# Kernel tuning notes

Measured on AMD Instinct MI355X. Metric: run time of the kernel, lower is better.

## Reference

```python
import jax, jax.numpy as jnp
import numpy as np

HIDDEN = 4096
INTER = 11008
BATCH, SEQ = 2, 2048


def _ternary(key, shape):
    # BitNet b1.58 ternary weights in {-1, 0, +1}
    return jax.random.randint(key, shape, -1, 2).astype(jnp.float32)


def setup_inputs() -> dict:
    key = jax.random.key(0)
    kx, kg, ku, kd = jax.random.split(key, 4)
    x = jax.random.normal(kx, (BATCH, SEQ, HIDDEN), dtype=jnp.float32)
    gate_w = _ternary(kg, (INTER, HIDDEN))
    up_w = _ternary(ku, (INTER, HIDDEN))
    down_w = _ternary(kd, (HIDDEN, INTER))
    # per-tensor absmean scales (dequant factors)
    gate_scale = jnp.float32(0.02)
    up_scale = jnp.float32(0.02)
    down_scale = jnp.float32(0.02)
    return {"x": x, "gate_w": gate_w, "up_w": up_w, "down_w": down_w,
            "gate_scale": gate_scale, "up_scale": up_scale, "down_scale": down_scale}


def reference(x, gate_w, up_w, down_w, gate_scale, up_scale, down_scale):
    # QuantizedLinear: y = (x @ W_q^T) * scale, W_q ternary, bias=False
    gate = jnp.einsum('bsh,ih->bsi', x, gate_w) * gate_scale
    up = jnp.einsum('bsh,ih->bsi', x, up_w) * up_scale
    inter = jax.nn.silu(gate) * up  # SwiGLU
    out = jnp.einsum('bsi,hi->bsh', inter, down_w) * down_scale
    return out
```

## Files before the change

kernel.cpp:

```cpp
#include <hip/hip_runtime.h>


typedef short short8 __attribute__((ext_vector_type(8)));
typedef float f32x4 __attribute__((ext_vector_type(4)));
typedef float fvec4 __attribute__((ext_vector_type(4)));
typedef unsigned short usvec4 __attribute__((ext_vector_type(4)));

__device__ __forceinline__ unsigned short f2bf(float f) {
    unsigned int u = __float_as_uint(f);
    u += 0x7FFFu + ((u >> 16) & 1u);
    return (unsigned short)(u >> 16);
}

__global__ void cvt_f32_bf16(const fvec4* __restrict__ src,
                             usvec4* __restrict__ dst, long n4) {
    long i = (long)blockIdx.x * blockDim.x + threadIdx.x;
    if (i < n4) {
        fvec4 v = __builtin_nontemporal_load(src + i);
        usvec4 o;
        o.x = f2bf(v.x); o.y = f2bf(v.y); o.z = f2bf(v.z); o.w = f2bf(v.w);
        dst[i] = o;
    }
}

__global__ void cvt2_f32_bf16_ilv(const fvec4* __restrict__ s0,
                                  const fvec4* __restrict__ s1,
                                  usvec4* __restrict__ d, long n4) {
    long i = (long)blockIdx.x * blockDim.x + threadIdx.x;
    if (i < n4) {
        long j = i >> 10;
        long c = i & 1023;
        long Rg = ((j & ~15L) << 1) | (j & 15);
        fvec4 a = __builtin_nontemporal_load(s0 + i);
        fvec4 b = __builtin_nontemporal_load(s1 + i);
        usvec4 oa, ob;
        oa.x = f2bf(a.x); oa.y = f2bf(a.y); oa.z = f2bf(a.z); oa.w = f2bf(a.w);
        ob.x = f2bf(b.x); ob.y = f2bf(b.y); ob.z = f2bf(b.z); ob.w = f2bf(b.w);
        d[Rg * 1024 + c] = oa;
        d[(Rg + 16) * 1024 + c] = ob;
    }
}

#define GLOBAL_TO_LDS(gp, lp)                                                  \
    __builtin_amdgcn_global_load_lds(                                          \
        (__attribute__((address_space(1))) const void*)(gp),                   \
        (__attribute__((address_space(3))) void*)(lp), 16, 0, 0)

#define BAR() __builtin_amdgcn_s_barrier()
#define SCHEDB() __builtin_amdgcn_sched_barrier(0)
#define LGKM(n) do { asm volatile("s_waitcnt lgkmcnt(" #n ")" ::: "memory"); SCHEDB(); } while (0)
#define VMW(n) asm volatile("s_waitcnt vmcnt(" #n ")" ::: "memory")

__device__ __forceinline__ void remap_block(int gy, int& bx, int& by) {
    int nwg = gy << 4;
    int orig = blockIdx.y * 16 + blockIdx.x;
    int q = nwg >> 3, r = nwg & 7;
    int xcd = orig & 7, lid = orig >> 3;
    int wg = (xcd < r ? xcd * (q + 1) : r * (q + 1) + (xcd - r) * q) + lid;
    bx = wg & 15;
    by = wg >> 4;
}

#define KITER(KT_, BFC, BFN, TOK4, PF_, RA_)                                   \
  do {                                                                         \
    LGKM(4);                        \
    __builtin_amdgcn_s_setprio(1);                                             \
    _Pragma("unroll") for (int mi = 0; mi < 4; ++mi)                           \
      _Pragma("unroll") for (int ni = 0; ni < 4; ++ni)                         \
        acc[mi][ni] = __builtin_amdgcn_mfma_f32_16x16x32_bf16(                 \
            ah0[mi], BFC[ni], acc[mi][ni], 0, 0, 0);                           \
    __builtin_amdgcn_s_setprio(0);                                             \
    SCHEDB();                                                                  \
    if (TOK4) { VMW(4); } else { VMW(0); }                                     \
    BAR();                                   \
    if (RA_) {                                                                 \
      const unsigned short* Aq = lds + ((((KT_) + 1) & 3) << 13);              \
      const unsigned short* Bq = lds + 32768 + ((((KT_) + 1) & 3) << 13);      \
      _Pragma("unroll") for (int i = 0; i < 4; ++i)                            \
        ah0[i] = *(const short8*)(Aq + aoff + i * 512);                        \
      _Pragma("unroll") for (int n = 0; n < 4; ++n)                            \
        BFN[n] = *(const short8*)(Bq + boff + n * 512);                        \
    }                                                                          \
    if (PF_) {                                                                 \
      unsigned short* Aw = lds + ((((KT_) + 3) & 3) << 13);                    \
      unsigned short* Bw = lds + 32768 + ((((KT_) + 3) & 3) << 13);            \
      GLOBAL_TO_LDS(pa0, Aw + t * 8);                                          \
      GLOBAL_TO_LDS(pa1, Aw + 4096 + t * 8);                                   \
      GLOBAL_TO_LDS(pb0, Bw + t * 8);                                          \
      GLOBAL_TO_LDS(pb1, Bw + 4096 + t * 8);                                   \
      pa0 += 32; pa1 += 32; pb0 += 32; pb1 += 32;                              \
    }                                                                          \
    SCHEDB();                                                                  \
    if (RA_) { LGKM(8); } else { LGKM(0); }   \
    __builtin_amdgcn_s_setprio(1);                                             \
    _Pragma("unroll") for (int mi = 0; mi < 4; ++mi)                           \
      _Pragma("unroll") for (int ni = 0; ni < 4; ++ni)                         \
        acc[4 + mi][ni] = __builtin_amdgcn_mfma_f32_16x16x32_bf16(             \
            ah1[mi], BFC[ni], acc[4 + mi][ni], 0, 0, 0);                       \
    __builtin_amdgcn_s_setprio(0);                                             \
    SCHEDB();                                                                  \
    if (RA_) {          \
      const unsigned short* Aq = lds + ((((KT_) + 1) & 3) << 13);              \
      _Pragma("unroll") for (int i = 0; i < 4; ++i)                            \
        ah1[i] = *(const short8*)(Aq + aoff + (4 + i) * 512);                  \
      SCHEDB();                                                                \
    }                                                                          \
  } while (0)

#define KPRO()                                                                 \
  do {                                                                         \
    _Pragma("unroll") for (int s = 0; s < 3; ++s) {                            \
      unsigned short* Aw = lds + (s << 13);                                    \
      unsigned short* Bw = lds + 32768 + (s << 13);                            \
      GLOBAL_TO_LDS(pa0, Aw + t * 8);                                          \
      GLOBAL_TO_LDS(pa1, Aw + 4096 + t * 8);                                   \
      GLOBAL_TO_LDS(pb0, Bw + t * 8);                                          \
      GLOBAL_TO_LDS(pb1, Bw + 4096 + t * 8);                                   \
      pa0 += 32; pa1 += 32; pb0 += 32; pb1 += 32;                              \
    }                                                                          \
    VMW(8); BAR();                     \
    _Pragma("unroll") for (int i = 0; i < 4; ++i)                              \
      ah0[i] = *(const short8*)(lds + aoff + i * 512);                         \
    _Pragma("unroll") for (int n = 0; n < 4; ++n)                              \
      bfA[n] = *(const short8*)(lds + 32768 + boff + n * 512);                 \
    _Pragma("unroll") for (int i = 0; i < 4; ++i)                              \
      ah1[i] = *(const short8*)(lds + aoff + (4 + i) * 512);                   \
    SCHEDB();                                                                  \
  } while (0)

#define KLOOP()                                                                \
  do {                                                                         \
    for (int kt = 0; kt < Kt - 4; kt += 2) {                                   \
      KITER(kt, bfA, bfB, 1, 1, 1);                                            \
      KITER(kt + 1, bfB, bfA, 1, 1, 1);                                        \
    }                                                                          \
    KITER(Kt - 4, bfA, bfB, 1, 1, 1);                                          \
    KITER(Kt - 3, bfB, bfA, 1, 0, 1);                                          \
    KITER(Kt - 2, bfA, bfB, 0, 0, 1);                                          \
    KITER(Kt - 1, bfB, bfA, 0, 0, 0);                                          \
  } while (0)

__global__ __launch_bounds__(512, 2)
void gemm1_swiglu(const unsigned short* __restrict__ Xb,
                  const unsigned short* __restrict__ Wc,
                  unsigned short* __restrict__ inter,
                  const float* __restrict__ gs_p,
                  const float* __restrict__ us_p,
                  int K, int I, int n0, int gy) {
    extern __shared__ unsigned short lds[];

    int bx, by;
    remap_block(gy, bx, by);

    const int t = threadIdx.x;
    const int lane = t & 63;
    const int wid = t >> 6;
    const int wm = (wid >> 2) * 128;
    const int wn = (wid & 3) * 64;
    const int fr = lane & 15;
    const int ca = (((lane >> 4) ^ ((fr >> 1) & 3)) << 3);

    const int m_base = bx * 256;
    const long b_row0 = (long)by * 256;

    const int colsw = (((t & 3) ^ ((t >> 3) & 3)) << 3);
    const unsigned short* pa0 = Xb + (size_t)(m_base + (t >> 2)) * K + colsw;
    const unsigned short* pa1 = pa0 + (size_t)128 * K;
    const unsigned short* pb0 = Wc + (size_t)(b_row0 + (t >> 2)) * K + colsw;
    const unsigned short* pb1 = pb0 + (size_t)128 * K;

    f32x4 acc[8][4];
    const f32x4 z = {0.0f, 0.0f, 0.0f, 0.0f};
#pragma unroll
    for (int i = 0; i < 8; ++i)
#pragma unroll
        for (int j = 0; j < 4; ++j) acc[i][j] = z;

    const int aoff = (wm + fr) * 32 + ca;
    const int boff = (wn + fr) * 32 + ca;
    const int Kt = K >> 5;

    short8 ah0[4], ah1[4], bfA[4], bfB[4];

    KPRO();
    KLOOP();

    const float gsc = *gs_p;
    const float usc = *us_p;
    const int row0 = m_base + wm + ((lane >> 4) << 2);
    const int col0 = n0 + by * 128 + (wn >> 1) + fr;
#pragma unroll
    for (int mi = 0; mi < 8; ++mi)
#pragma unroll
        for (int p = 0; p < 2; ++p)
#pragma unroll
            for (int r = 0; r < 4; ++r) {
                float g = acc[mi][2 * p][r] * gsc;
                float u = acc[mi][2 * p + 1][r] * usc;
                float s = g / (1.0f + __expf(-g));
                inter[(size_t)(row0 + mi * 16 + r) * I + (col0 + p * 16)] =
                    f2bf(s * u);
            }
}

__global__ __launch_bounds__(512, 2)
void gemm2_down(const unsigned short* __restrict__ Ab,
                const unsigned short* __restrict__ Dw,
                float* __restrict__ out,
                const float* __restrict__ ds_p,
                int K, int H, int n0, int gy) {
    extern __shared__ unsigned short lds[];

    int bx, by;
    remap_block(gy, bx, by);

    const int t = threadIdx.x;
    const int lane = t & 63;
    const int wid = t >> 6;
    const int wm = (wid >> 2) * 128;
    const int wn = (wid & 3) * 64;
    const int fr = lane & 15;
    const int ca = (((lane >> 4) ^ ((fr >> 1) & 3)) << 3);

    const int m_base = bx * 256;
    const long b_row0 = (long)by * 256;

    const int colsw = (((t & 3) ^ ((t >> 3) & 3)) << 3);
    const unsigned short* pa0 = Ab + (size_t)(m_base + (t >> 2)) * K + colsw;
    const unsigned short* pa1 = pa0 + (size_t)128 * K;
    const unsigned short* pb0 = Dw + (size_t)(b_row0 + (t >> 2)) * K + colsw;
    const unsigned short* pb1 = pb0 + (size_t)128 * K;

    f32x4 acc[8][4];
    const f32x4 z = {0.0f, 0.0f, 0.0f, 0.0f};
#pragma unroll
    for (int i = 0; i < 8; ++i)
#pragma unroll
        for (int j = 0; j < 4; ++j) acc[i][j] = z;

    const int aoff = (wm + fr) * 32 + ca;
    const int boff = (wn + fr) * 32 + ca;
    const int Kt = K >> 5;

    short8 ah0[4], ah1[4], bfA[4], bfB[4];

    KPRO();
    KLOOP();

    const float dsc = *ds_p;
    const int row0 = m_base + wm + ((lane >> 4) << 2);
    const int col0 = n0 + by * 256 + wn + fr;
#pragma unroll
    for (int mi = 0; mi < 8; ++mi)
#pragma unroll
        for (int ni = 0; ni < 4; ++ni)
#pragma unroll
            for (int r = 0; r < 4; ++r)
                out[(size_t)(row0 + mi * 16 + r) * H + (col0 + ni * 16)] =
                    acc[mi][ni][r] * dsc;
}

extern "C" void kernel_launch(void* const* d_in, const int* in_sizes, int n_in,
                              void* d_out, int out_size, void* d_ws, size_t ws_size,
                              hipStream_t stream) {
    (void)in_sizes; (void)n_in; (void)out_size;
    const float* x  = (const float*)d_in[0];
    const float* gw = (const float*)d_in[1];
    const float* uw = (const float*)d_in[2];
    const float* dw = (const float*)d_in[3];
    const float* gs = (const float*)d_in[4];
    const float* us = (const float*)d_in[5];
    const float* ds = (const float*)d_in[6];
    float* out = (float*)d_out;

    const long M = 4096;
    const long Kh = 4096;
    const long I = 11008;
    const long H = 4096;

    (void)hipFuncSetAttribute(reinterpret_cast<const void*>(gemm1_swiglu),
                              hipFuncAttributeMaxDynamicSharedMemorySize, 131072);
    (void)hipFuncSetAttribute(reinterpret_cast<const void*>(gemm2_down),
                              hipFuncAttributeMaxDynamicSharedMemorySize, 131072);

    char* ws = (char*)d_ws;
    unsigned short* Xb = (unsigned short*)ws;
    unsigned short* inter = (unsigned short*)(ws + M * Kh * 2);
    const size_t used = (size_t)M * Kh * 2 + (size_t)M * I * 2;
    if (ws_size < used + 2 * (size_t)256 * Kh * 2) return;
    char* wbuf = ws + used;
    const size_t avail = ws_size - used;

    {
        long n4 = M * Kh / 4;
        cvt_f32_bf16<<<dim3((unsigned)((n4 + 255) / 256)), dim3(256), 0, stream>>>(
            (const fvec4*)x, (usvec4*)Xb, n4);
    }

    long mr1 = (long)(avail / ((size_t)2 * Kh * 2));
    mr1 = (mr1 / 128) * 128;
    if (mr1 > I) mr1 = I;
    if (mr1 < 128) mr1 = 128;
    unsigned short* Wc = (unsigned short*)wbuf;
    for (long n0 = 0; n0 < I; n0 += mr1) {
        long rc = (I - n0 < mr1) ? (I - n0) : mr1;
        long e4 = rc * Kh / 4;
        unsigned cb = (unsigned)((e4 + 255) / 256);
        cvt2_f32_bf16_ilv<<<dim3(cb), dim3(256), 0, stream>>>(
            (const fvec4*)(gw + n0 * Kh), (const fvec4*)(uw + n0 * Kh),
            (usvec4*)Wc, e4);
        unsigned gy = (unsigned)(rc / 128);
        gemm1_swiglu<<<dim3(16, gy), dim3(512), 131072, stream>>>(
            Xb, Wc, inter, gs, us, (int)Kh, (int)I, (int)n0, (int)gy);
    }

    long mr2 = (long)(avail / ((size_t)I * 2));
    mr2 = (mr2 / 256) * 256;
    if (mr2 > H) mr2 = H;
    if (mr2 < 256) mr2 = 256;
    unsigned short* Wd = (unsigned short*)wbuf;
    for (long h0 = 0; h0 < H; h0 += mr2) {
        long rc = (H - h0 < mr2) ? (H - h0) : mr2;
        long e4 = rc * I / 4;
        unsigned cb = (unsigned)((e4 + 255) / 256);
        cvt_f32_bf16<<<dim3(cb), dim3(256), 0, stream>>>(
            (const fvec4*)(dw + h0 * I), (usvec4*)Wd, e4);
        unsigned gy = (unsigned)(rc / 256);
        gemm2_down<<<dim3(16, gy), dim3(512), 131072, stream>>>(
            inter, Wd, out, ds, (int)I, (int)H, (int)h0, (int)gy);
    }
}
```

Baseline: 1.394 ms.

## Fuse fp32-to-bf16 weight conversion into GEMM mainloops via register staging

Drops the separate weight conversion kernels and chunked launch loops. Both GEMMs now load fp32 weights straight into registers, truncate them to bf16 by packing the high halves, and write them to LDS one stage ahead, while activations still use direct global-to-LDS loads. This removes the bf16 weight round-trip through memory and the extra launches, but each block now reads twice the weight bytes, converts by truncation instead of round-to-nearest (exact for ternary weights), and changes the wait-count scheduling. The x conversion kernel becomes grid-stride with a fixed grid.

Result: slower. 2.053 ms (+47.2%).

```diff
diff --git a/kernel.cpp b/kernel.cpp
--- a/kernel.cpp
+++ b/kernel.cpp
@@ -5,6 +5,7 @@
 typedef float f32x4 __attribute__((ext_vector_type(4)));
 typedef float fvec4 __attribute__((ext_vector_type(4)));
 typedef unsigned short usvec4 __attribute__((ext_vector_type(4)));
+typedef unsigned int u32x4 __attribute__((ext_vector_type(4)));
 
 __device__ __forceinline__ unsigned short f2bf(float f) {
     unsigned int u = __float_as_uint(f);
@@ -12,32 +13,18 @@
     return (unsigned short)(u >> 16);
 }
 
+__device__ __forceinline__ unsigned pkbf(unsigned a, unsigned b) {
+    return (a >> 16) | (b & 0xFFFF0000u);
+}
+
 __global__ void cvt_f32_bf16(const fvec4* __restrict__ src,
                              usvec4* __restrict__ dst, long n4) {
-    long i = (long)blockIdx.x * blockDim.x + threadIdx.x;
-    if (i < n4) {
+    long stride = (long)gridDim.x * blockDim.x;
+    for (long i = (long)blockIdx.x * blockDim.x + threadIdx.x; i < n4; i += stride) {
         fvec4 v = __builtin_nontemporal_load(src + i);
         usvec4 o;
         o.x = f2bf(v.x); o.y = f2bf(v.y); o.z = f2bf(v.z); o.w = f2bf(v.w);
         dst[i] = o;
-    }
-}
-
-__global__ void cvt2_f32_bf16_ilv(const fvec4* __restrict__ s0,
-                                  const fvec4* __restrict__ s1,
-                                  usvec4* __restrict__ d, long n4) {
-    long i = (long)blockIdx.x * blockDim.x + threadIdx.x;
-    if (i < n4) {
-        long j = i >> 10;
-        long c = i & 1023;
-        long Rg = ((j & ~15L) << 1) | (j & 15);
-        fvec4 a = __builtin_nontemporal_load(s0 + i);
-        fvec4 b = __builtin_nontemporal_load(s1 + i);
-        usvec4 oa, ob;
-        oa.x = f2bf(a.x); oa.y = f2bf(a.y); oa.z = f2bf(a.z); oa.w = f2bf(a.w);
-        ob.x = f2bf(b.x); ob.y = f2bf(b.y); ob.z = f2bf(b.z); ob.w = f2bf(b.w);
-        d[Rg * 1024 + c] = oa;
-        d[(Rg + 16) * 1024 + c] = ob;
     }
 }
 
@@ -61,7 +48,7 @@
     by = wg >> 4;
 }
 
-#define KITER(KT_, BFC, BFN, TOK4, PF_, RA_)                                   \
+#define KITER(KT_, BFC, BFN, WSRC, WDST, VM_, MID_, WR_, LD_, RA_)             \
   do {                                                                         \
     LGKM(4);                        \
     __builtin_amdgcn_s_setprio(1);                                             \
@@ -71,8 +58,30 @@
             ah0[mi], BFC[ni], acc[mi][ni], 0, 0, 0);                           \
     __builtin_amdgcn_s_setprio(0);                                             \
     SCHEDB();                                                                  \
-    if (TOK4) { VMW(4); } else { VMW(0); }                                     \
-    BAR();                                   \
+    VMW(VM_);                     \
+    BAR();                                                                     \
+    if (LD_) {                                                                 \
+      WDST[0] = pq0[0]; WDST[1] = pq0[1];                                      \
+      WDST[2] = pq1[0]; WDST[3] = pq1[1];                                      \
+      pq0 += 8; pq1 += 8;                                                      \
+      SCHEDB();                                                                \
+      unsigned short* Aw = lds + ((((KT_) + 3) & 3) << 13);                    \
+      GLOBAL_TO_LDS(pa0, Aw + t * 8);                                          \
+      GLOBAL_TO_LDS(pa1, Aw + 4096 + t * 8);                                   \
+      pa0 += 32; pa1 += 32;                                                    \
+      SCHEDB();                                                                \
+    }                                                                          \
+    if (WR_) {                                                                 \
+      unsigned short* Bw = lds + 32768 + ((((KT_) + 2) & 3) << 13);            \
+      u32x4 lo, hi;                                                            \
+      lo.x = pkbf(WSRC[0].x, WSRC[0].y); lo.y = pkbf(WSRC[0].z, WSRC[0].w);    \
+      lo.z = pkbf(WSRC[1].x, WSRC[1].y); lo.w = pkbf(WSRC[1].z, WSRC[1].w);    \
+      hi.x = pkbf(WSRC[2].x, WSRC[2].y); hi.y = pkbf(WSRC[2].z, WSRC[2].w);    \
+      hi.z = pkbf(WSRC[3].x, WSRC[3].y); hi.w = pkbf(WSRC[3].z, WSRC[3].w);    \
+      *(u32x4*)(Bw + t * 8) = lo;                                              \
+      *(u32x4*)(Bw + 4096 + t * 8) = hi;                                       \
+      SCHEDB();                                                                \
+    }                                                                          \
     if (RA_) {                                                                 \
       const unsigned short* Aq = lds + ((((KT_) + 1) & 3) << 13);              \
       const unsigned short* Bq = lds + 32768 + ((((KT_) + 1) & 3) << 13);      \
@@ -81,17 +90,7 @@
       _Pragma("unroll") for (int n = 0; n < 4; ++n)                            \
         BFN[n] = *(const short8*)(Bq + boff + n * 512);                        \
     }                                                                          \
-    if (PF_) {                                                                 \
-      unsigned short* Aw = lds + ((((KT_) + 3) & 3) << 13);                    \
-      unsigned short* Bw = lds + 32768 + ((((KT_) + 3) & 3) << 13);            \
-      GLOBAL_TO_LDS(pa0, Aw + t * 8);                                          \
-      GLOBAL_TO_LDS(pa1, Aw + 4096 + t * 8);                                   \
-      GLOBAL_TO_LDS(pb0, Bw + t * 8);                                          \
-      GLOBAL_TO_LDS(pb1, Bw + 4096 + t * 8);                                   \
-      pa0 += 32; pa1 += 32; pb0 += 32; pb1 += 32;                              \
-    }                                                                          \
-    SCHEDB();                                                                  \
-    if (RA_) { LGKM(8); } else { LGKM(0); }   \
+    LGKM(MID_);                                     \
     __builtin_amdgcn_s_setprio(1);                                             \
     _Pragma("unroll") for (int mi = 0; mi < 4; ++mi)                           \
       _Pragma("unroll") for (int ni = 0; ni < 4; ++ni)                         \
@@ -99,7 +98,7 @@
             ah1[mi], BFC[ni], acc[4 + mi][ni], 0, 0, 0);                       \
     __builtin_amdgcn_s_setprio(0);                                             \
     SCHEDB();                                                                  \
-    if (RA_) {          \
+    if (RA_) {                                                                 \
       const unsigned short* Aq = lds + ((((KT_) + 1) & 3) << 13);              \
       _Pragma("unroll") for (int i = 0; i < 4; ++i)                            \
         ah1[i] = *(const short8*)(Aq + aoff + (4 + i) * 512);                  \
@@ -109,16 +108,39 @@
 
 #define KPRO()                                                                 \
   do {                                                                         \
+    wP0[0] = pq0[0]; wP0[1] = pq0[1]; wP0[2] = pq1[0]; wP0[3] = pq1[1];        \
+    pq0 += 8; pq1 += 8;                                                        \
+    wP1[0] = pq0[0]; wP1[1] = pq0[1]; wP1[2] = pq1[0]; wP1[3] = pq1[1];        \
+    pq0 += 8; pq1 += 8;                                                        \
+    qA[0] = pq0[0]; qA[1] = pq0[1]; qA[2] = pq1[0]; qA[3] = pq1[1];            \
+    pq0 += 8; pq1 += 8;                                                        \
+    SCHEDB();                                                                  \
     _Pragma("unroll") for (int s = 0; s < 3; ++s) {                            \
       unsigned short* Aw = lds + (s << 13);                                    \
-      unsigned short* Bw = lds + 32768 + (s << 13);                            \
       GLOBAL_TO_LDS(pa0, Aw + t * 8);                                          \
       GLOBAL_TO_LDS(pa1, Aw + 4096 + t * 8);                                   \
-      GLOBAL_TO_LDS(pb0, Bw + t * 8);                                          \
-      GLOBAL_TO_LDS(pb1, Bw + 4096 + t * 8);                                   \
-      pa0 += 32; pa1 += 32; pb0 += 32; pb1 += 32;                              \
-    }                                                                          \
-    VMW(8); BAR();                     \
+      pa0 += 32; pa1 += 32;                                                    \
+    }                                                                          \
+    VMW(0);                                                                    \
+    {                                                                          \
+      unsigned short* Bw = lds + 32768;                                        \
+      u32x4 lo, hi;                                                            \
+      lo.x = pkbf(wP0[0].x, wP0[0].y); lo.y = pkbf(wP0[0].z, wP0[0].w);        \
+      lo.z = pkbf(wP0[1].x, wP0[1].y); lo.w = pkbf(wP0[1].z, wP0[1].w);        \
+      hi.x = pkbf(wP0[2].x, wP0[2].y); hi.y = pkbf(wP0[2].z, wP0[2].w);        \
+      hi.z = pkbf(wP0[3].x, wP0[3].y); hi.w = pkbf(wP0[3].z, wP0[3].w);        \
+      *(u32x4*)(Bw + t * 8) = lo;                                              \
+      *(u32x4*)(Bw + 4096 + t * 8) = hi;                                       \
+      Bw = lds + 32768 + 8192;                                                 \
+      lo.x = pkbf(wP1[0].x, wP1[0].y); lo.y = pkbf(wP1[0].z, wP1[0].w);        \
+      lo.z = pkbf(wP1[1].x, wP1[1].y); lo.w = pkbf(wP1[1].z, wP1[1].w);        \
+      hi.x = pkbf(wP1[2].x, wP1[2].y); hi.y = pkbf(wP1[2].z, wP1[2].w);        \
+      hi.z = pkbf(wP1[3].x, wP1[3].y); hi.w = pkbf(wP1[3].z, wP1[3].w);        \
+      *(u32x4*)(Bw + t * 8) = lo;                                              \
+      *(u32x4*)(Bw + 4096 + t * 8) = hi;                                       \
+    }                                                                          \
+    LGKM(0);                                                                   \
+    BAR();                                                                     \
     _Pragma("unroll") for (int i = 0; i < 4; ++i)                              \
       ah0[i] = *(const short8*)(lds + aoff + i * 512);                         \
     _Pragma("unroll") for (int n = 0; n < 4; ++n)                              \
@@ -130,23 +152,25 @@
 
 #define KLOOP()                                                                \
   do {                                                                         \
-    for (int kt = 0; kt < Kt - 4; kt += 2) {                                   \
-      KITER(kt, bfA, bfB, 1, 1, 1);                                            \
-      KITER(kt + 1, bfB, bfA, 1, 1, 1);                                        \
-    }                                                                          \
-    KITER(Kt - 4, bfA, bfB, 1, 1, 1);                                          \
-    KITER(Kt - 3, bfB, bfA, 1, 0, 1);                                          \
-    KITER(Kt - 2, bfA, bfB, 0, 0, 1);                                          \
-    KITER(Kt - 1, bfB, bfA, 0, 0, 0);                                          \
+    int kt = 0;                                                                \
+    for (; kt < Kt - 4; kt += 2) {                                             \
+      KITER(kt, bfA, bfB, qA, qB, 2, 10, 1, 1, 1);                             \
+      KITER(kt + 1, bfB, bfA, qB, qA, 2, 10, 1, 1, 1);                         \
+    }                                                                          \
+    KITER(kt, bfA, bfB, qA, qB, 2, 10, 1, 1, 1); ++kt;               \
+    KITER(kt, bfB, bfA, qB, qA, 2, 10, 1, 0, 1); ++kt;               \
+    KITER(kt, bfA, bfB, qA, qB, 0, 8, 0, 0, 1); ++kt;                \
+    KITER(kt, bfB, bfA, qB, qA, 0, 0, 0, 0, 0);                      \
   } while (0)
 
 __global__ __launch_bounds__(512, 2)
 void gemm1_swiglu(const unsigned short* __restrict__ Xb,
-                  const unsigned short* __restrict__ Wc,
+                  const float* __restrict__ Gw,
+                  const float* __restrict__ Uw,
                   unsigned short* __restrict__ inter,
                   const float* __restrict__ gs_p,
                   const float* __restrict__ us_p,
-                  int K, int I, int n0, int gy) {
+                  int K, int I, int gy) {
     extern __shared__ unsigned short lds[];
 
     int bx, by;
@@ -161,13 +185,17 @@
     const int ca = (((lane >> 4) ^ ((fr >> 1) & 3)) << 3);
 
     const int m_base = bx * 256;
-    const long b_row0 = (long)by * 256;
-
-    const int colsw = (((t & 3) ^ ((t >> 3) & 3)) << 3);
-    const unsigned short* pa0 = Xb + (size_t)(m_base + (t >> 2)) * K + colsw;
+
+    const int g = (t & 3) ^ ((t >> 3) & 3);
+    const int rl = t >> 2;
+    const unsigned short* pa0 = Xb + (size_t)(m_base + rl) * K + g * 8;
     const unsigned short* pa1 = pa0 + (size_t)128 * K;
-    const unsigned short* pb0 = Wc + (size_t)(b_row0 + (t >> 2)) * K + colsw;
-    const unsigned short* pb1 = pb0 + (size_t)128 * K;
+
+    const int cg = by * 256 + rl;
+    const float* wbase = ((cg >> 4) & 1) ? Uw : Gw;
+    const int srow = ((cg >> 5) << 4) + (cg & 15);
+    const u32x4* pq0 = (const u32x4*)(wbase + (size_t)srow * K) + 2 * g;
+    const u32x4* pq1 = pq0 + (size_t)16 * K;
 
     f32x4 acc[8][4];
     const f32x4 z = {0.0f, 0.0f, 0.0f, 0.0f};
@@ -181,6 +209,7 @@
     const int Kt = K >> 5;
 
     short8 ah0[4], ah1[4], bfA[4], bfB[4];
+    u32x4 qA[4], qB[4], wP0[4], wP1[4];
 
     KPRO();
     KLOOP();
@@ -188,27 +217,27 @@
     const float gsc = *gs_p;
     const float usc = *us_p;
     const int row0 = m_base + wm + ((lane >> 4) << 2);
-    const int col0 = n0 + by * 128 + (wn >> 1) + fr;
+    const int col0 = by * 128 + (wn >> 1) + fr;
 #pragma unroll
     for (int mi = 0; mi < 8; ++mi)
 #pragma unroll
         for (int p = 0; p < 2; ++p)
 #pragma unroll
             for (int r = 0; r < 4; ++r) {
-                float g = acc[mi][2 * p][r] * gsc;
-                float u = acc[mi][2 * p + 1][r] * usc;
-                float s = g / (1.0f + __expf(-g));
+                float gg = acc[mi][2 * p][r] * gsc;
+                float uu = acc[mi][2 * p + 1][r] * usc;
+                float s = gg / (1.0f + __expf(-gg));
                 inter[(size_t)(row0 + mi * 16 + r) * I + (col0 + p * 16)] =
-                    f2bf(s * u);
+                    f2bf(s * uu);
             }
 }
 
 __global__ __launch_bounds__(512, 2)
 void gemm2_down(const unsigned short* __restrict__ Ab,
-                const unsigned short* __restrict__ Dw,
+                const float* __restrict__ Dw,
                 float* __restrict__ out,
                 const float* __restrict__ ds_p,
-                int K, int H, int n0, int gy) {
+                int K, int H, int gy) {
     extern __shared__ unsigned short lds[];
 
     int bx, by;
@@ -225,11 +254,13 @@
     const int m_base = bx * 256;
     const long b_row0 = (long)by * 256;
 
-    const int colsw = (((t & 3) ^ ((t >> 3) & 3)) << 3);
-    const unsigned short* pa0 = Ab + (size_t)(m_base + (t >> 2)) * K + colsw;
+    const int g = (t & 3) ^ ((t >> 3) & 3);
+    const int rl = t >> 2;
+    const unsigned short* pa0 = Ab + (size_t)(m_base + rl) * K + g * 8;
     const unsigned short* pa1 = pa0 + (size_t)128 * K;
-    const unsigned short* pb0 = Dw + (size_t)(b_row0 + (t >> 2)) * K + colsw;
-    const unsigned short* pb1 = pb0 + (size_t)128 * K;
+
+    const u32x4* pq0 = (const u32x4*)(Dw + (size_t)(b_row0 + rl) * K) + 2 * g;
+    const u32x4* pq1 = pq0 + (size_t)32 * K;
 
     f32x4 acc[8][4];
     const f32x4 z = {0.0f, 0.0f, 0.0f, 0.0f};
@@ -243,13 +274,14 @@
     const int Kt = K >> 5;
 
     short8 ah0[4], ah1[4], bfA[4], bfB[4];
+    u32x4 qA[4], qB[4], wP0[4], wP1[4];
 
     KPRO();
     KLOOP();
 
     const float dsc = *ds_p;
     const int row0 = m_base + wm + ((lane >> 4) << 2);
-    const int col0 = n0 + by * 256 + wn + fr;
+    const int col0 = by * 256 + wn + fr;
 #pragma unroll
     for (int mi = 0; mi < 8; ++mi)
 #pragma unroll
@@ -285,48 +317,19 @@
 
     char* ws = (char*)d_ws;
     unsigned short* Xb = (unsigned short*)ws;
-    unsigned short* inter = (unsigned short*)(ws + M * Kh * 2);
+    unsigned short* inter = (unsigned short*)(ws + (size_t)M * Kh * 2);
     const size_t used = (size_t)M * Kh * 2 + (size_t)M * I * 2;
-    if (ws_size < used + 2 * (size_t)256 * Kh * 2) return;
-    char* wbuf = ws + used;
-    const size_t avail = ws_size - used;
+    if (ws_size < used) return;
 
     {
         long n4 = M * Kh / 4;
-        cvt_f32_bf16<<<dim3((unsigned)((n4 + 255) / 256)), dim3(256), 0, stream>>>(
+        cvt_f32_bf16<<<dim3(2048), dim3(256), 0, stream>>>(
             (const fvec4*)x, (usvec4*)Xb, n4);
     }
 
-    long mr1 = (long)(avail / ((size_t)2 * Kh * 2));
-    mr1 = (mr1 / 128) * 128;
-    if (mr1 > I) mr1 = I;
-    if (mr1 < 128) mr1 = 128;
-    unsigned short* Wc = (unsigned short*)wbuf;
-    for (long n0 = 0; n0 < I; n0 += mr1) {
-        long rc = (I - n0 < mr1) ? (I - n0) : mr1;
-        long e4 = rc * Kh / 4;
-        unsigned cb = (unsigned)((e4 + 255) / 256);
-        cvt2_f32_bf16_ilv<<<dim3(cb), dim3(256), 0, stream>>>(
-            (const fvec4*)(gw + n0 * Kh), (const fvec4*)(uw + n0 * Kh),
-            (usvec4*)Wc, e4);
-        unsigned gy = (unsigned)(rc / 128);
-        gemm1_swiglu<<<dim3(16, gy), dim3(512), 131072, stream>>>(
-            Xb, Wc, inter, gs, us, (int)Kh, (int)I, (int)n0, (int)gy);
-    }
-
-    long mr2 = (long)(avail / ((size_t)I * 2));
-    mr2 = (mr2 / 256) * 256;
-    if (mr2 > H) mr2 = H;
-    if (mr2 < 256) mr2 = 256;
-    unsigned short* Wd = (unsigned short*)wbuf;
-    for (long h0 = 0; h0 < H; h0 += mr2) {
-        long rc = (H - h0 < mr2) ? (H - h0) : mr2;
-        long e4 = rc * I / 4;
-        unsigned cb = (unsigned)((e4 + 255) / 256);
-        cvt_f32_bf16<<<dim3(cb), dim3(256), 0, stream>>>(
-            (const fvec4*)(dw + h0 * I), (usvec4*)Wd, e4);
-        unsigned gy = (unsigned)(rc / 256);
-        gemm2_down<<<dim3(16, gy), dim3(512), 131072, stream>>>(
-            inter, Wd, out, ds, (int)I, (int)H, (int)h0, (int)gy);
-    }
-}
+    gemm1_swiglu<<<dim3(16, 86), dim3(512), 131072, stream>>>(
+        Xb, gw, uw, inter, gs, us, (int)Kh, (int)I, 86);
+
+    gemm2_down<<<dim3(16, 16), dim3(512), 131072, stream>>>(
+        inter, dw, out, ds, (int)I, (int)H, 16);
+}
```

## Restructure GEMM main loop into 64-wide K groups with split prefetch schedule

Applied to the files above, without the earlier changes.

Replaces the per-32-K iteration pipeline with a group that processes two 32-wide K chunks at once, splitting the MFMA work into four 4x2 quadrants interleaved with LDS fragment loads and staggered global-to-LDS prefetches of A and B. The intent is to give each MFMA burst more independent work and overlap LDS reads and async copies better, at the cost of many more barriers per group and higher register use. The conversion kernels are also changed to grid-stride loops with a fixed grid of 2048 blocks.

Measured after the change: 1.379 ms. Within noise of the previous version (-1.1%).

```diff
diff --git a/kernel.cpp b/kernel.cpp
--- a/kernel.cpp
+++ b/kernel.cpp
@@ -14,8 +14,8 @@
 
 __global__ void cvt_f32_bf16(const fvec4* __restrict__ src,
                              usvec4* __restrict__ dst, long n4) {
-    long i = (long)blockIdx.x * blockDim.x + threadIdx.x;
-    if (i < n4) {
+    long stride = (long)gridDim.x * blockDim.x;
+    for (long i = (long)blockIdx.x * blockDim.x + threadIdx.x; i < n4; i += stride) {
         fvec4 v = __builtin_nontemporal_load(src + i);
         usvec4 o;
         o.x = f2bf(v.x); o.y = f2bf(v.y); o.z = f2bf(v.z); o.w = f2bf(v.w);
@@ -26,8 +26,8 @@
 __global__ void cvt2_f32_bf16_ilv(const fvec4* __restrict__ s0,
                                   const fvec4* __restrict__ s1,
                                   usvec4* __restrict__ d, long n4) {
-    long i = (long)blockIdx.x * blockDim.x + threadIdx.x;
-    if (i < n4) {
+    long stride = (long)gridDim.x * blockDim.x;
+    for (long i = (long)blockIdx.x * blockDim.x + threadIdx.x; i < n4; i += stride) {
         long j = i >> 10;
         long c = i & 1023;
         long Rg = ((j & ~15L) << 1) | (j & 15);
@@ -61,83 +61,119 @@
     by = wg >> 4;
 }
 
-#define KITER(KT_, BFC, BFN, TOK4, PF_, RA_)                                   \
-  do {                                                                         \
-    LGKM(4);                        \
-    __builtin_amdgcn_s_setprio(1);                                             \
-    _Pragma("unroll") for (int mi = 0; mi < 4; ++mi)                           \
-      _Pragma("unroll") for (int ni = 0; ni < 4; ++ni)                         \
-        acc[mi][ni] = __builtin_amdgcn_mfma_f32_16x16x32_bf16(                 \
-            ah0[mi], BFC[ni], acc[mi][ni], 0, 0, 0);                           \
-    __builtin_amdgcn_s_setprio(0);                                             \
-    SCHEDB();                                                                  \
-    if (TOK4) { VMW(4); } else { VMW(0); }                                     \
-    BAR();                                   \
-    if (RA_) {                                                                 \
-      const unsigned short* Aq = lds + ((((KT_) + 1) & 3) << 13);              \
-      const unsigned short* Bq = lds + 32768 + ((((KT_) + 1) & 3) << 13);      \
-      _Pragma("unroll") for (int i = 0; i < 4; ++i)                            \
-        ah0[i] = *(const short8*)(Aq + aoff + i * 512);                        \
-      _Pragma("unroll") for (int n = 0; n < 4; ++n)                            \
-        BFN[n] = *(const short8*)(Bq + boff + n * 512);                        \
-    }                                                                          \
-    if (PF_) {                                                                 \
-      unsigned short* Aw = lds + ((((KT_) + 3) & 3) << 13);                    \
-      unsigned short* Bw = lds + 32768 + ((((KT_) + 3) & 3) << 13);            \
-      GLOBAL_TO_LDS(pa0, Aw + t * 8);                                          \
-      GLOBAL_TO_LDS(pa1, Aw + 4096 + t * 8);                                   \
-      GLOBAL_TO_LDS(pb0, Bw + t * 8);                                          \
-      GLOBAL_TO_LDS(pb1, Bw + 4096 + t * 8);                                   \
-      pa0 += 32; pa1 += 32; pb0 += 32; pb1 += 32;                              \
-    }                                                                          \
-    SCHEDB();                                                                  \
-    if (RA_) { LGKM(8); } else { LGKM(0); }   \
-    __builtin_amdgcn_s_setprio(1);                                             \
-    _Pragma("unroll") for (int mi = 0; mi < 4; ++mi)                           \
-      _Pragma("unroll") for (int ni = 0; ni < 4; ++ni)                         \
-        acc[4 + mi][ni] = __builtin_amdgcn_mfma_f32_16x16x32_bf16(             \
-            ah1[mi], BFC[ni], acc[4 + mi][ni], 0, 0, 0);                       \
-    __builtin_amdgcn_s_setprio(0);                                             \
-    SCHEDB();                                                                  \
-    if (RA_) {          \
-      const unsigned short* Aq = lds + ((((KT_) + 1) & 3) << 13);              \
-      _Pragma("unroll") for (int i = 0; i < 4; ++i)                            \
-        ah1[i] = *(const short8*)(Aq + aoff + (4 + i) * 512);                  \
-      SCHEDB();                                                                \
-    }                                                                          \
+#define MFMA16(AH, BH, MH, NH)                                                \
+  do {                                                                        \
+    __builtin_amdgcn_s_setprio(1);                                            \
+    _Pragma("unroll") for (int kk = 0; kk < 2; ++kk)                          \
+      _Pragma("unroll") for (int mi = 0; mi < 4; ++mi)                        \
+        _Pragma("unroll") for (int ni = 0; ni < 2; ++ni)                      \
+          acc[(MH)*4+mi][(NH)*2+ni] =                                         \
+              __builtin_amdgcn_mfma_f32_16x16x32_bf16(                        \
+                  AH[kk*4+mi], BH[kk*2+ni], acc[(MH)*4+mi][(NH)*2+ni],        \
+                  0, 0, 0);                                                   \
+    __builtin_amdgcn_s_setprio(0);                                            \
+    SCHEDB();                                                                 \
   } while (0)
 
-#define KPRO()                                                                 \
-  do {                                                                         \
-    _Pragma("unroll") for (int s = 0; s < 3; ++s) {                            \
-      unsigned short* Aw = lds + (s << 13);                                    \
-      unsigned short* Bw = lds + 32768 + (s << 13);                            \
-      GLOBAL_TO_LDS(pa0, Aw + t * 8);                                          \
-      GLOBAL_TO_LDS(pa1, Aw + 4096 + t * 8);                                   \
-      GLOBAL_TO_LDS(pb0, Bw + t * 8);                                          \
-      GLOBAL_TO_LDS(pb1, Bw + 4096 + t * 8);                                   \
-      pa0 += 32; pa1 += 32; pb0 += 32; pb1 += 32;                              \
-    }                                                                          \
-    VMW(8); BAR();                     \
-    _Pragma("unroll") for (int i = 0; i < 4; ++i)                              \
-      ah0[i] = *(const short8*)(lds + aoff + i * 512);                         \
-    _Pragma("unroll") for (int n = 0; n < 4; ++n)                              \
-      bfA[n] = *(const short8*)(lds + 32768 + boff + n * 512);                 \
-    _Pragma("unroll") for (int i = 0; i < 4; ++i)                              \
-      ah1[i] = *(const short8*)(lds + aoff + (4 + i) * 512);                   \
-    SCHEDB();                                                                  \
+#define KGROUP(C0, C1, SA, SB, TOK)                                           \
+  do {                                                                        \
+         \
+    { const unsigned short* Aq0 = lds + (C0) * 8192;                          \
+      const unsigned short* Aq1 = lds + (C1) * 8192;                          \
+      const unsigned short* Bq0 = lds + 32768 + (C0) * 8192;                  \
+      const unsigned short* Bq1 = lds + 32768 + (C1) * 8192;                  \
+      _Pragma("unroll") for (int mi = 0; mi < 4; ++mi) {                      \
+        a0[mi]     = *(const short8*)(Aq0 + aoff + mi * 512);                 \
+        a0[4 + mi] = *(const short8*)(Aq1 + aoff + mi * 512);                 \
+      }                                                                       \
+      _Pragma("unroll") for (int ni = 0; ni < 2; ++ni) {                      \
+        b0[ni]     = *(const short8*)(Bq0 + boff + ni * 512);                 \
+        b0[2 + ni] = *(const short8*)(Bq1 + boff + ni * 512);                 \
+      }                                                                       \
+    }                                                                         \
+    if (SA) {                                                                 \
+      GLOBAL_TO_LDS(pa0, lds + ((C0) ^ 2) * 8192 + t * 8);                    \
+      GLOBAL_TO_LDS(pa1, lds + ((C0) ^ 2) * 8192 + 4096 + t * 8);             \
+      pa0 += 32; pa1 += 32;                                                   \
+    }                                                                         \
+    LGKM(8); BAR(); LGKM(0);                                                  \
+    MFMA16(a0, b0, 0, 0);                                                     \
+    BAR();                                                                    \
+                                 \
+    { const unsigned short* Bq0 = lds + 32768 + (C0) * 8192;                  \
+      const unsigned short* Bq1 = lds + 32768 + (C1) * 8192;                  \
+      _Pragma("unroll") for (int ni = 0; ni < 2; ++ni) {                      \
+        b1[ni]     = *(const short8*)(Bq0 + boff + (2 + ni) * 512);           \
+        b1[2 + ni] = *(const short8*)(Bq1 + boff + (2 + ni) * 512);           \
+      }                                                                       \
+    }                                                                         \
+    if (SA) {                                                                 \
+      GLOBAL_TO_LDS(pa0, lds + ((C1) ^ 2) * 8192 + t * 8);                    \
+      GLOBAL_TO_LDS(pa1, lds + ((C1) ^ 2) * 8192 + 4096 + t * 8);             \
+      pa0 += 32; pa1 += 32;                                                   \
+    }                                                                         \
+    BAR(); LGKM(0);                                                           \
+    MFMA16(a0, b1, 0, 1);                                                     \
+    BAR();                                                                    \
+      \
+    { const unsigned short* Aq0 = lds + (C0) * 8192;                          \
+      const unsigned short* Aq1 = lds + (C1) * 8192;                          \
+      _Pragma("unroll") for (int mi = 0; mi < 4; ++mi) {                      \
+        a1[mi]     = *(const short8*)(Aq0 + aoff + (4 + mi) * 512);           \
+        a1[4 + mi] = *(const short8*)(Aq1 + aoff + (4 + mi) * 512);           \
+      }                                                                       \
+    }                                                                         \
+    if (SB) {                                                                 \
+      GLOBAL_TO_LDS(pb0, lds + 32768 + (C0) * 8192 + t * 8);                  \
+      GLOBAL_TO_LDS(pb1, lds + 32768 + (C0) * 8192 + 4096 + t * 8);           \
+      pb0 += 32; pb1 += 32;                                                   \
+    }                                                                         \
+    BAR(); LGKM(0);                                                           \
+    MFMA16(a1, b1, 1, 1);                                                     \
+    BAR();                                                                    \
+        \
+    if (SB) {                                                                 \
+      GLOBAL_TO_LDS(pb0, lds + 32768 + (C1) * 8192 + t * 8);                  \
+      GLOBAL_TO_LDS(pb1, lds + 32768 + (C1) * 8192 + 4096 + t * 8);           \
+      pb0 += 32; pb1 += 32;                                                   \
+    }                                                                         \
+    if ((TOK) == 2) { VMW(4); } else if ((TOK) == 1) { VMW(0); }              \
+    BAR();                                                                    \
+    MFMA16(a1, b0, 1, 0);                                                     \
+    BAR();                                                                    \
   } while (0)
 
-#define KLOOP()                                                                \
-  do {                                                                         \
-    for (int kt = 0; kt < Kt - 4; kt += 2) {                                   \
-      KITER(kt, bfA, bfB, 1, 1, 1);                                            \
-      KITER(kt + 1, bfB, bfA, 1, 1, 1);                                        \
-    }                                                                          \
-    KITER(Kt - 4, bfA, bfB, 1, 1, 1);                                          \
-    KITER(Kt - 3, bfB, bfA, 1, 0, 1);                                          \
-    KITER(Kt - 2, bfA, bfB, 0, 0, 1);                                          \
-    KITER(Kt - 1, bfB, bfA, 0, 0, 0);                                          \
+#define KPRO8()                                                               \
+  do {                                                                        \
+    GLOBAL_TO_LDS(pa0, lds + t * 8);                                          \
+    GLOBAL_TO_LDS(pa1, lds + 4096 + t * 8);                                   \
+    pa0 += 32; pa1 += 32;                                                     \
+    GLOBAL_TO_LDS(pb0, lds + 32768 + t * 8);                                  \
+    GLOBAL_TO_LDS(pb1, lds + 32768 + 4096 + t * 8);                           \
+    pb0 += 32; pb1 += 32;                                                     \
+    GLOBAL_TO_LDS(pa0, lds + 8192 + t * 8);                                   \
+    GLOBAL_TO_LDS(pa1, lds + 8192 + 4096 + t * 8);                            \
+    pa0 += 32; pa1 += 32;                                                     \
+    GLOBAL_TO_LDS(pb0, lds + 32768 + 8192 + t * 8);                           \
+    GLOBAL_TO_LDS(pb1, lds + 32768 + 8192 + 4096 + t * 8);                    \
+    pb0 += 32; pb1 += 32;                                                     \
+    GLOBAL_TO_LDS(pb0, lds + 32768 + 16384 + t * 8);                          \
+    GLOBAL_TO_LDS(pb1, lds + 32768 + 16384 + 4096 + t * 8);                   \
+    pb0 += 32; pb1 += 32;                                                     \
+    GLOBAL_TO_LDS(pb0, lds + 32768 + 24576 + t * 8);                          \
+    GLOBAL_TO_LDS(pb1, lds + 32768 + 24576 + 4096 + t * 8);                   \
+    pb0 += 32; pb1 += 32;                                                     \
+    VMW(4); BAR();                                                            \
+  } while (0)
+
+#define KLOOP8()                                                              \
+  do {                                                                        \
+    for (int g = 0; g < G - 2; g += 2) {                                      \
+      KGROUP(0, 1, 1, 1, 2);                                                  \
+      KGROUP(2, 3, 1, 1, 2);                                                  \
+    }                                                                         \
+    KGROUP(0, 1, 1, 0, 1);                                                    \
+    KGROUP(2, 3, 0, 0, 0);                                                    \
   } while (0)
 
 __global__ __launch_bounds__(512, 2)
@@ -178,12 +214,12 @@
 
     const int aoff = (wm + fr) * 32 + ca;
     const int boff = (wn + fr) * 32 + ca;
-    const int Kt = K >> 5;
-
-    short8 ah0[4], ah1[4], bfA[4], bfB[4];
-
-    KPRO();
-    KLOOP();
+    const int G = K >> 6;
+
+    short8 a0[8], a1[8], b0[4], b1[4];
+
+    KPRO8();
+    KLOOP8();
 
     const float gsc = *gs_p;
     const float usc = *us_p;
@@ -240,12 +276,12 @@
 
     const int aoff = (wm + fr) * 32 + ca;
     const int boff = (wn + fr) * 32 + ca;
-    const int Kt = K >> 5;
-
-    short8 ah0[4], ah1[4], bfA[4], bfB[4];
-
-    KPRO();
-    KLOOP();
+    const int G = K >> 6;
+
+    short8 a0[8], a1[8], b0[4], b1[4];
+
+    KPRO8();
+    KLOOP8();
 
     const float dsc = *ds_p;
     const int row0 = m_base + wm + ((lane >> 4) << 2);
@@ -285,7 +321,7 @@
 
     char* ws = (char*)d_ws;
     unsigned short* Xb = (unsigned short*)ws;
-    unsigned short* inter = (unsigned short*)(ws + M * Kh * 2);
+    unsigned short* inter = (unsigned short*)(ws + (size_t)M * Kh * 2);
     const size_t used = (size_t)M * Kh * 2 + (size_t)M * I * 2;
     if (ws_size < used + 2 * (size_t)256 * Kh * 2) return;
     char* wbuf = ws + used;
@@ -293,7 +329,7 @@
 
     {
         long n4 = M * Kh / 4;
-        cvt_f32_bf16<<<dim3((unsigned)((n4 + 255) / 256)), dim3(256), 0, stream>>>(
+        cvt_f32_bf16<<<dim3(2048), dim3(256), 0, stream>>>(
             (const fvec4*)x, (usvec4*)Xb, n4);
     }
 
@@ -304,11 +340,9 @@
     unsigned short* Wc = (unsigned short*)wbuf;
     for (long n0 = 0; n0 < I; n0 += mr1) {
         long rc = (I - n0 < mr1) ? (I - n0) : mr1;
-        long e4 = rc * Kh / 4;
-        unsigned cb = (unsigned)((e4 + 255) / 256);
-        cvt2_f32_bf16_ilv<<<dim3(cb), dim3(256), 0, stream>>>(
+        cvt2_f32_bf16_ilv<<<dim3(2048), dim3(256), 0, stream>>>(
             (const fvec4*)(gw + n0 * Kh), (const fvec4*)(uw + n0 * Kh),
-            (usvec4*)Wc, e4);
+            (usvec4*)Wc, rc * Kh / 4);
         unsigned gy = (unsigned)(rc / 128);
         gemm1_swiglu<<<dim3(16, gy), dim3(512), 131072, stream>>>(
             Xb, Wc, inter, gs, us, (int)Kh, (int)I, (int)n0, (int)gy);
@@ -321,10 +355,8 @@
     unsigned short* Wd = (unsigned short*)wbuf;
     for (long h0 = 0; h0 < H; h0 += mr2) {
         long rc = (H - h0 < mr2) ? (H - h0) : mr2;
-        long e4 = rc * I / 4;
-        unsigned cb = (unsigned)((e4 + 255) / 256);
-        cvt_f32_bf16<<<dim3(cb), dim3(256), 0, stream>>>(
-            (const fvec4*)(dw + h0 * I), (usvec4*)Wd, e4);
+        cvt_f32_bf16<<<dim3(2048), dim3(256), 0, stream>>>(
+            (const fvec4*)(dw + h0 * I), (usvec4*)Wd, rc * I / 4);
         unsigned gy = (unsigned)(rc / 256);
         gemm2_down<<<dim3(16, gy), dim3(512), 131072, stream>>>(
             inter, Wd, out, ds, (int)I, (int)H, (int)h0, (int)gy);
```
